# Performance work log

Hardware: AMD Instinct MI355X
Metric: run time of the kernel (lower is better)

The kernel has to match this reference:

```python
import jax, jax.numpy as jnp
from jax import lax
import numpy as np

EPS = 1e-5


def setup_inputs() -> dict:
    key = jax.random.key(0)
    ks = jax.random.split(key, 16)
    N, C, H, W = 8, 128, 128, 128
    MIP, OUP, K = 8, 128, 3
    inp = {}
    inp["x"] = jax.random.normal(ks[0], (N, C, H, W), dtype=jnp.float32)
    # conv1: 1x1, C -> MIP
    inp["w1"] = jax.random.normal(ks[1], (MIP, C), dtype=jnp.float32) * (1.0 / np.sqrt(C))
    inp["b1"] = jax.random.normal(ks[2], (MIP,), dtype=jnp.float32) * 0.02
    # bn1 (inference: frozen running stats)
    inp["g1"] = jnp.ones((MIP,), jnp.float32) + jax.random.normal(ks[3], (MIP,), jnp.float32) * 0.02
    inp["be1"] = jax.random.normal(ks[4], (MIP,), jnp.float32) * 0.02
    inp["m1"] = jax.random.normal(ks[5], (MIP,), jnp.float32) * 0.02
    inp["v1"] = jnp.ones((MIP,), jnp.float32)
    # conv_h / conv_w: 1x1, MIP -> C
    inp["wh"] = jax.random.normal(ks[6], (C, MIP), dtype=jnp.float32) * (1.0 / np.sqrt(MIP))
    inp["bh"] = jax.random.normal(ks[7], (C,), dtype=jnp.float32) * 0.02
    inp["ww"] = jax.random.normal(ks[8], (C, MIP), dtype=jnp.float32) * (1.0 / np.sqrt(MIP))
    inp["bw"] = jax.random.normal(ks[9], (C,), dtype=jnp.float32) * 0.02
    # final conv: KxK, C -> OUP
    inp["wc"] = jax.random.normal(ks[10], (OUP, C, K, K), dtype=jnp.float32) * (1.0 / np.sqrt(C * K * K))
    inp["bc"] = jax.random.normal(ks[11], (OUP,), dtype=jnp.float32) * 0.02
    inp["g2"] = jnp.ones((OUP,), jnp.float32) + jax.random.normal(ks[12], (OUP,), jnp.float32) * 0.02
    inp["be2"] = jax.random.normal(ks[13], (OUP,), jnp.float32) * 0.02
    inp["m2"] = jax.random.normal(ks[14], (OUP,), jnp.float32) * 0.02
    inp["v2"] = jnp.ones((OUP,), jnp.float32)
    return inp


def _bn1d(y, g, b, m, v):
    # y: (n, c, l); per-channel affine with frozen stats
    s = g / jnp.sqrt(v + EPS)
    return y * s[None, :, None] + (b - m * s)[None, :, None]


def _h_swish(y):
    return y * jnp.clip(y + 3.0, 0.0, 6.0) / 6.0


def reference(x, w1, b1, g1, be1, m1, v1, wh, bh, ww, bw, wc, bc, g2, be2, m2, v2):
    n, c, h, w = x.shape
    # Multi-scale pooled descriptors. Nearest interp of the 2-bin and 4-bin
    # adaptive pools back to length-1 picks bin 0, i.e. the mean over the
    # first half / first quarter of the pooled axis.
    x_h = x.mean(3) + x[..., : w // 2].mean(3) + x[..., : w // 4].mean(3)        # (n,c,h)
    x_w = x.mean(2) + x[:, :, : h // 2].mean(2) + x[:, :, : h // 4].mean(2)      # (n,c,w)
    y = jnp.concatenate([x_h, x_w], axis=2)                                       # (n,c,h+w)
    y = jnp.einsum('ncl,mc->nml', y, w1) + b1[None, :, None]                      # 1x1 conv
    y = _h_swish(_bn1d(y, g1, be1, m1, v1))
    xh, xw = y[:, :, :h], y[:, :, h:]
    a_h = jax.nn.sigmoid(jnp.einsum('nml,cm->ncl', xh, wh) + bh[None, :, None])[:, :, :, None]  # (n,c,h,1)
    a_w = jax.nn.sigmoid(jnp.einsum('nml,cm->ncl', xw, ww) + bw[None, :, None])[:, :, None, :]  # (n,c,1,w)
    out = x * a_w * a_h                                                           # gated features
    # final conv (kernel 3, stride 1, pad 1) + BN + SiLU
    out = lax.conv_general_dilated(out, wc, window_strides=(1, 1),
                                   padding=[(1, 1), (1, 1)],
                                   dimension_numbers=('NCHW', 'OIHW', 'NCHW'))
    out = out + bc[None, :, None, None]
    s2 = g2 / jnp.sqrt(v2 + EPS)
    out = out * s2[None, :, None, None] + (be2 - m2 * s2)[None, :, None, None]
    return out * jax.nn.sigmoid(out)
```

## Files before the change

kernel.cpp:

```cpp
#include <hip/hip_runtime.h>
#include <hip/hip_bf16.h>

typedef float f32x4 __attribute__((ext_vector_type(4)));
typedef __bf16 bf16x8 __attribute__((ext_vector_type(8)));

#define EPSF 1e-5f

__device__ __forceinline__ float pw(int i) {
    return (1.0f + (i < 64 ? 2.0f : 0.0f) + (i < 32 ? 4.0f : 0.0f)) * (1.0f / 128.0f);
}

__global__ __launch_bounds__(256) void pool_kernel(const float* __restrict__ x,
                                                   float* __restrict__ P) {
    int nc = blockIdx.x;
    const f32x4* plane = (const f32x4*)(x + (size_t)nc * 16384);
    __shared__ float rowpart[128][33];
    __shared__ __align__(16) f32x4 colpart[8][32];
    int t = threadIdx.x;
    int wq = t & 31, hg = t >> 5;
    f32x4 cacc = {0.f, 0.f, 0.f, 0.f};
    float u0 = pw(wq * 4), u1 = pw(wq * 4 + 1), u2 = pw(wq * 4 + 2), u3 = pw(wq * 4 + 3);
    #pragma unroll
    for (int j = 0; j < 16; ++j) {
        int r = hg * 16 + j;
        f32x4 v = plane[r * 32 + wq];
        rowpart[r][wq] = v.x * u0 + v.y * u1 + v.z * u2 + v.w * u3;
        cacc += v * pw(r);
    }
    colpart[hg][wq] = cacc;
    __syncthreads();
    float s = 0.f;
    if (t < 128) {
        #pragma unroll
        for (int q = 0; q < 32; ++q) s += rowpart[t][q];
        P[(size_t)nc * 256 + t] = s;
    } else {
        int w = t - 128;
        const float* cp = (const float*)colpart;
        #pragma unroll
        for (int g = 0; g < 8; ++g) s += cp[g * 128 + w];
        P[(size_t)nc * 256 + 128 + w] = s;
    }
}

__global__ __launch_bounds__(256) void attn_kernel(const float* __restrict__ P,
    const float* __restrict__ w1, const float* __restrict__ b1,
    const float* __restrict__ g1, const float* __restrict__ be1,
    const float* __restrict__ m1, const float* __restrict__ v1,
    const float* __restrict__ wh, const float* __restrict__ bh,
    const float* __restrict__ ww, const float* __restrict__ bw,
    float* __restrict__ A2) {
    int n = blockIdx.x >> 2, cg = blockIdx.x & 3, t = threadIdx.x;
    __shared__ float w1s[1024], whs[256], wws[256];
    __shared__ float bhs[32], bws[32];
    __shared__ float s1[8], t1[8], b1s[8];
    for (int i = t; i < 1024; i += 256) w1s[i] = w1[i];
    whs[t] = wh[cg * 256 + t];
    wws[t] = ww[cg * 256 + t];
    if (t < 32) { bhs[t] = bh[cg * 32 + t]; bws[t] = bw[cg * 32 + t]; }
    if (t < 8) {
        float s = g1[t] * rsqrtf(v1[t] + EPSF);
        s1[t] = s; t1[t] = be1[t] - m1[t] * s; b1s[t] = b1[t];
    }
    __syncthreads();
    float y[8];
    #pragma unroll
    for (int m = 0; m < 8; ++m) y[m] = b1s[m];
    const float* Pn = P + (size_t)n * 32768;
    for (int c = 0; c < 128; ++c) {
        float pv = Pn[c * 256 + t];
        #pragma unroll
        for (int m = 0; m < 8; ++m) y[m] += w1s[m * 128 + c] * pv;
    }
    #pragma unroll
    for (int m = 0; m < 8; ++m) {
        float v = y[m] * s1[m] + t1[m];
        float cl = fminf(fmaxf(v + 3.f, 0.f), 6.f);
        y[m] = v * cl * (1.f / 6.f);
    }
    const float* Ws_ = (t < 128) ? whs : wws;
    const float* Bs = (t < 128) ? bhs : bws;
    float* On = A2 + (size_t)n * 32768;
    for (int cc = 0; cc < 32; ++cc) {
        int c = cg * 32 + cc;
        float a = Bs[cc];
        #pragma unroll
        for (int m = 0; m < 8; ++m) a += y[m] * Ws_[cc * 8 + m];
        On[c * 256 + t] = 1.f / (1.f + __expf(-a));
    }
}

__global__ __launch_bounds__(256) void wtrans_kernel(const float* __restrict__ wc,
    const float* __restrict__ bc, const float* __restrict__ g2, const float* __restrict__ be2,
    const float* __restrict__ m2, const float* __restrict__ v2,
    __hip_bfloat16* __restrict__ Wt, float* __restrict__ ab) {
    int g = blockIdx.x * 256 + threadIdx.x;
    int step = g >> 12, rem = g & 4095;
    int o = rem >> 5, m = rem & 31;
    int slotp = m >> 3, j = m & 7;
    int u = slotp ^ ((o >> 1) & 3);
    int kidx = u * 8 + j;
    int khw = step >> 2, c32 = step & 3;
    int c = c32 * 32 + kidx;
    Wt[g] = __float2bfloat16(wc[(o * 128 + c) * 9 + khw]);
    if (g < 128) {
        float s2 = g2[g] * rsqrtf(v2[g] + EPSF);
        ab[g] = s2;
        ab[128 + g] = bc[g] * s2 + be2[g] - m2[g] * s2;
    }
}

__device__ __forceinline__ int ldsoff(int w, int c) {
    return w * 128 + ((((c >> 3) ^ ((w & 7) << 1)) << 3) | (c & 7));
}

__global__ __launch_bounds__(256) void amul_kernel(const float* __restrict__ x,
    const float* __restrict__ A2, __hip_bfloat16* __restrict__ Xpad) {
    int nh = blockIdx.x;
    int n = nh >> 7, h = nh & 127;
    int t = threadIdx.x;
    __shared__ __align__(16) __hip_bfloat16 T[16384];
    __shared__ float ahs[128];
    if (t < 128) ahs[t] = A2[(size_t)(n * 128 + t) * 256 + h];

    uint4 z = {0u, 0u, 0u, 0u};
    __hip_bfloat16* Xn = Xpad + (size_t)n * 16900 * 128;
    if (t < 32) {
        int wp = (t & 1) ? 129 : 0, cb2 = t >> 1;
        *(uint4*)(Xn + (size_t)((h + 1) * 130 + wp) * 128 + cb2 * 8) = z;
    }
    if (h == 0 || h == 127) {
        int hp = (h == 0) ? 0 : 129;
        for (int i = t; i < 2080; i += 256) {
            int wp = i >> 4, cb2 = i & 15;
            *(uint4*)(Xn + (size_t)(hp * 130 + wp) * 128 + cb2 * 8) = z;
        }
    }
    __syncthreads();

    const float* xr  = x + ((size_t)n * 128 * 128 + h) * 128;
    const float* awr = A2 + (size_t)n * 32768 + 128;
    #pragma unroll
    for (int j = 0; j < 16; ++j) {
        int item = j * 256 + t;
        int c = item >> 5, w4 = item & 31;
        f32x4 xv = *(const f32x4*)(xr + (size_t)c * 16384 + w4 * 4);
        f32x4 av = *(const f32x4*)(awr + c * 256 + w4 * 4);
        float ah = ahs[c];
        #pragma unroll
        for (int k = 0; k < 4; ++k) {
            float val = xv[k] * av[k] * ah;
            T[ldsoff(w4 * 4 + k, c)] = __float2bfloat16(val);
        }
    }
    __syncthreads();
    __hip_bfloat16* orow = Xn + (size_t)((h + 1) * 130 + 1) * 128;
    #pragma unroll
    for (int j = 0; j < 8; ++j) {
        int item = j * 256 + t;
        int w = item >> 4, cb = item & 15;
        int slot = cb ^ ((w & 7) << 1);
        uint4 v = *(const uint4*)&T[w * 128 + slot * 8];
        *(uint4*)(orow + w * 128 + cb * 8) = v;
    }
}

__global__ __launch_bounds__(512, 4) void conv_kernel(
    const __hip_bfloat16* __restrict__ Xpad, const __hip_bfloat16* __restrict__ Wt,
    const float* __restrict__ ab, float* __restrict__ out) {
    int bid = blockIdx.x;
    int work = (bid & 7) * 64 + (bid >> 3);
    int n = work >> 6, h0 = (work & 63) * 2;
    int tid = threadIdx.x;
    int lane = tid & 63, wid = tid >> 6;
    int wm = wid >> 2, wn = wid & 3;
    int r16 = lane & 15, u = lane >> 4;

    __shared__ __align__(16) __hip_bfloat16 Ws[3 * 4096];
    __shared__ __align__(16) __hip_bfloat16 Xs[3 * 8192];

    const __hip_bfloat16* Xn = Xpad + ((size_t)n * 16900 + (size_t)h0 * 130) * 128;

    int offA[4], offB[4];
    #pragma unroll
    for (int mi = 0; mi < 4; ++mi) {
        int o = wm * 64 + mi * 16 + r16;
        offA[mi] = o * 32 + ((u ^ ((o >> 1) & 3)) << 3);
    }
    #pragma unroll
    for (int ni = 0; ni < 4; ++ni) {
        int p = wn * 64 + ni * 16 + r16;
        offB[ni] = p * 32 + ((u ^ ((p >> 1) & 3)) << 3);
    }

    int xo[2];
    #pragma unroll
    for (int j = 0; j < 2; ++j) {
        int idx = j * 512 + tid, p = idx >> 2, s = idx & 3;
        int r2 = p >> 7, w = p & 127;
        xo[j] = (r2 * 130 + w) * 128 + ((s ^ ((p >> 1) & 3)) << 3);
    }

    auto stage = [&](int t) {
        int khw = t >> 2, c32 = t & 3;
        int kh = khw / 3, kw = khw - kh * 3;
        __builtin_amdgcn_global_load_lds(
            (const __attribute__((address_space(1))) void*)(Wt + t * 4096 + tid * 8),
            (__attribute__((address_space(3))) void*)(&Ws[(t % 3) * 4096 + tid * 8]),
            16, 0, 0);
        const __hip_bfloat16* xsrc = Xn + (kh * 130 + kw) * 128 + c32 * 32;
        __hip_bfloat16* xdst = &Xs[(t % 3) * 8192];
        #pragma unroll
        for (int j = 0; j < 2; ++j)
            __builtin_amdgcn_global_load_lds(
                (const __attribute__((address_space(1))) void*)(xsrc + xo[j]),
                (__attribute__((address_space(3))) void*)(xdst + (j * 512 + tid) * 8),
                16, 0, 0);
    };

    f32x4 acc[4][4];
    #pragma unroll
    for (int i = 0; i < 4; ++i)
        #pragma unroll
        for (int j = 0; j < 4; ++j) acc[i][j] = (f32x4){0.f, 0.f, 0.f, 0.f};

    stage(0);
    stage(1);
    asm volatile("s_waitcnt vmcnt(3)" ::: "memory");
    __builtin_amdgcn_sched_barrier(0);
    __builtin_amdgcn_s_barrier();
    __builtin_amdgcn_sched_barrier(0);

    #pragma unroll
    for (int t = 0; t < 36; ++t) {
        const __hip_bfloat16* Wb = &Ws[(t % 3) * 4096];
        const __hip_bfloat16* Xr = &Xs[(t % 3) * 8192];
        if (t + 2 < 36) stage(t + 2);

        bf16x8 xa[4], xb[4];
        #pragma unroll
        for (int mi = 0; mi < 4; ++mi) xa[mi] = *(const bf16x8*)&Wb[offA[mi]];
        #pragma unroll
        for (int ni = 0; ni < 4; ++ni) xb[ni] = *(const bf16x8*)&Xr[offB[ni]];
        asm volatile("s_waitcnt lgkmcnt(0)" ::: "memory");
        __builtin_amdgcn_sched_barrier(0);
        __builtin_amdgcn_s_setprio(1);
        #pragma unroll
        for (int mi = 0; mi < 4; ++mi)
            #pragma unroll
            for (int ni = 0; ni < 4; ++ni)
                acc[mi][ni] = __builtin_amdgcn_mfma_f32_16x16x32_bf16(
                    xa[mi], xb[ni], acc[mi][ni], 0, 0, 0);
        __builtin_amdgcn_s_setprio(0);

        if (t < 34) {
            asm volatile("s_waitcnt vmcnt(3)" ::: "memory");
        } else if (t == 34) {
            asm volatile("s_waitcnt vmcnt(0)" ::: "memory");
        }
        __builtin_amdgcn_sched_barrier(0);
        if (t < 35) {
            __builtin_amdgcn_s_barrier();
            __builtin_amdgcn_sched_barrier(0);
        }
    }

    #pragma unroll
    for (int mi = 0; mi < 4; ++mi) {
        #pragma unroll
        for (int r = 0; r < 4; ++r) {
            int o = wm * 64 + mi * 16 + u * 4 + r;
            float al = ab[o], be = ab[128 + o];
            size_t obase = (((size_t)n * 128 + o) * 128 + h0) * 128;
            #pragma unroll
            for (int ni = 0; ni < 4; ++ni) {
                int p = wn * 64 + ni * 16 + r16;
                int r2 = p >> 7, w = p & 127;
                float z = acc[mi][ni][r] * al + be;
                out[obase + r2 * 128 + w] = z / (1.f + __expf(-z));
            }
        }
    }
}

extern "C" void kernel_launch(void* const* d_in, const int* in_sizes, int n_in,
                              void* d_out, int out_size, void* d_ws, size_t ws_size,
                              hipStream_t stream) {
    const float* x   = (const float*)d_in[0];
    const float* w1  = (const float*)d_in[1];
    const float* b1  = (const float*)d_in[2];
    const float* g1  = (const float*)d_in[3];
    const float* be1 = (const float*)d_in[4];
    const float* m1  = (const float*)d_in[5];
    const float* v1  = (const float*)d_in[6];
    const float* wh  = (const float*)d_in[7];
    const float* bh  = (const float*)d_in[8];
    const float* ww  = (const float*)d_in[9];
    const float* bw  = (const float*)d_in[10];
    const float* wc  = (const float*)d_in[11];
    const float* bc  = (const float*)d_in[12];
    const float* g2  = (const float*)d_in[13];
    const float* be2 = (const float*)d_in[14];
    const float* m2  = (const float*)d_in[15];
    const float* v2  = (const float*)d_in[16];
    float* out = (float*)d_out;

    char* ws = (char*)d_ws;
    float* P  = (float*)(ws);
    float* A2 = (float*)(ws + (1 << 20));
    __hip_bfloat16* Xpad = (__hip_bfloat16*)(ws + (2 << 20));
    __hip_bfloat16* Wt   = (__hip_bfloat16*)(ws + (2 << 20) + 34611200);
    float* ab = (float*)(ws + (2 << 20) + 34611200 + 294912);

    pool_kernel<<<1024, 256, 0, stream>>>(x, P);
    attn_kernel<<<32, 256, 0, stream>>>(P, w1, b1, g1, be1, m1, v1, wh, bh, ww, bw, A2);
    wtrans_kernel<<<576, 256, 0, stream>>>(wc, bc, g2, be2, m2, v2, Wt, ab);
    amul_kernel<<<1024, 256, 0, stream>>>(x, A2, Xpad);
    conv_kernel<<<512, 512, 0, stream>>>(Xpad, Wt, ab, out);
}
```

Baseline: 110.0 us.

## Merge attn and weight-transform kernels; enlarge per-wave conv tile to 128x64

The conv kernel now runs 4 waves per block instead of 8, and each wave computes all 128 output channels for a 64-pixel slice. This doubles A-fragment register reuse and halves LDS fragment reads per MFMA, at the cost of more accumulator registers (128 VGPRs of acc) and fewer waves for latency hiding. Each thread also issues twice as many global-to-LDS loads, and the vmcnt waits are adjusted to match. Separately, the attention and weight-transform kernels are merged into one launch with a block-index split, removing one kernel launch.

```diff
diff --git a/kernel.cpp b/kernel.cpp
--- a/kernel.cpp
+++ b/kernel.cpp
@@ -43,14 +43,35 @@
     }
 }
 
-__global__ __launch_bounds__(256) void attn_kernel(const float* __restrict__ P,
+__global__ __launch_bounds__(256) void attn_wtrans_kernel(const float* __restrict__ P,
     const float* __restrict__ w1, const float* __restrict__ b1,
     const float* __restrict__ g1, const float* __restrict__ be1,
     const float* __restrict__ m1, const float* __restrict__ v1,
     const float* __restrict__ wh, const float* __restrict__ bh,
     const float* __restrict__ ww, const float* __restrict__ bw,
-    float* __restrict__ A2) {
-    int n = blockIdx.x >> 2, cg = blockIdx.x & 3, t = threadIdx.x;
+    const float* __restrict__ wc, const float* __restrict__ bc,
+    const float* __restrict__ g2, const float* __restrict__ be2,
+    const float* __restrict__ m2, const float* __restrict__ v2,
+    float* __restrict__ A2, __hip_bfloat16* __restrict__ Wt, float* __restrict__ ab) {
+    int t = threadIdx.x;
+    if (blockIdx.x >= 32) {
+        int g = (blockIdx.x - 32) * 256 + t;
+        int step = g >> 12, rem = g & 4095;
+        int o = rem >> 5, m = rem & 31;
+        int slotp = m >> 3, j = m & 7;
+        int u = slotp ^ ((o >> 1) & 3);
+        int kidx = u * 8 + j;
+        int khw = step >> 2, c32 = step & 3;
+        int c = c32 * 32 + kidx;
+        Wt[g] = __float2bfloat16(wc[(o * 128 + c) * 9 + khw]);
+        if (g < 128) {
+            float s2 = g2[g] * rsqrtf(v2[g] + EPSF);
+            ab[g] = s2;
+            ab[128 + g] = bc[g] * s2 + be2[g] - m2[g] * s2;
+        }
+        return;
+    }
+    int n = blockIdx.x >> 2, cg = blockIdx.x & 3;
     __shared__ float w1s[1024], whs[256], wws[256];
     __shared__ float bhs[32], bws[32];
     __shared__ float s1[8], t1[8], b1s[8];
@@ -90,26 +111,6 @@
     }
 }
 
-__global__ __launch_bounds__(256) void wtrans_kernel(const float* __restrict__ wc,
-    const float* __restrict__ bc, const float* __restrict__ g2, const float* __restrict__ be2,
-    const float* __restrict__ m2, const float* __restrict__ v2,
-    __hip_bfloat16* __restrict__ Wt, float* __restrict__ ab) {
-    int g = blockIdx.x * 256 + threadIdx.x;
-    int step = g >> 12, rem = g & 4095;
-    int o = rem >> 5, m = rem & 31;
-    int slotp = m >> 3, j = m & 7;
-    int u = slotp ^ ((o >> 1) & 3);
-    int kidx = u * 8 + j;
-    int khw = step >> 2, c32 = step & 3;
-    int c = c32 * 32 + kidx;
-    Wt[g] = __float2bfloat16(wc[(o * 128 + c) * 9 + khw]);
-    if (g < 128) {
-        float s2 = g2[g] * rsqrtf(v2[g] + EPSF);
-        ab[g] = s2;
-        ab[128 + g] = bc[g] * s2 + be2[g] - m2[g] * s2;
-    }
-}
-
 __device__ __forceinline__ int ldsoff(int w, int c) {
     return w * 128 + ((((c >> 3) ^ ((w & 7) << 1)) << 3) | (c & 7));
 }
@@ -165,15 +166,15 @@
     }
 }
 
-__global__ __launch_bounds__(512, 4) void conv_kernel(
+__global__ __launch_bounds__(256, 2) void conv_kernel(
     const __hip_bfloat16* __restrict__ Xpad, const __hip_bfloat16* __restrict__ Wt,
     const float* __restrict__ ab, float* __restrict__ out) {
     int bid = blockIdx.x;
     int work = (bid & 7) * 64 + (bid >> 3);
     int n = work >> 6, h0 = (work & 63) * 2;
     int tid = threadIdx.x;
-    int lane = tid & 63, wid = tid >> 6;
-    int wm = wid >> 2, wn = wid & 3;
+    int lane = tid & 63;
+    int wn = tid >> 6;
     int r16 = lane & 15, u = lane >> 4;
 
     __shared__ __align__(16) __hip_bfloat16 Ws[3 * 4096];
@@ -181,10 +182,10 @@
 
     const __hip_bfloat16* Xn = Xpad + ((size_t)n * 16900 + (size_t)h0 * 130) * 128;
 
-    int offA[4], offB[4];
-    #pragma unroll
-    for (int mi = 0; mi < 4; ++mi) {
-        int o = wm * 64 + mi * 16 + r16;
+    int offA[8], offB[4];
+    #pragma unroll
+    for (int mi = 0; mi < 8; ++mi) {
+        int o = mi * 16 + r16;
         offA[mi] = o * 32 + ((u ^ ((o >> 1) & 3)) << 3);
     }
     #pragma unroll
@@ -193,10 +194,10 @@
         offB[ni] = p * 32 + ((u ^ ((p >> 1) & 3)) << 3);
     }
 
-    int xo[2];
-    #pragma unroll
-    for (int j = 0; j < 2; ++j) {
-        int idx = j * 512 + tid, p = idx >> 2, s = idx & 3;
+    int xo[4];
+    #pragma unroll
+    for (int j = 0; j < 4; ++j) {
+        int idx = j * 256 + tid, p = idx >> 2, s = idx & 3;
         int r2 = p >> 7, w = p & 127;
         xo[j] = (r2 * 130 + w) * 128 + ((s ^ ((p >> 1) & 3)) << 3);
     }
@@ -204,29 +205,31 @@
     auto stage = [&](int t) {
         int khw = t >> 2, c32 = t & 3;
         int kh = khw / 3, kw = khw - kh * 3;
-        __builtin_amdgcn_global_load_lds(
-            (const __attribute__((address_space(1))) void*)(Wt + t * 4096 + tid * 8),
-            (__attribute__((address_space(3))) void*)(&Ws[(t % 3) * 4096 + tid * 8]),
-            16, 0, 0);
+        #pragma unroll
+        for (int j = 0; j < 2; ++j)
+            __builtin_amdgcn_global_load_lds(
+                (const __attribute__((address_space(1))) void*)(Wt + t * 4096 + (j * 256 + tid) * 8),
+                (__attribute__((address_space(3))) void*)(&Ws[(t % 3) * 4096 + (j * 256 + tid) * 8]),
+                16, 0, 0);
         const __hip_bfloat16* xsrc = Xn + (kh * 130 + kw) * 128 + c32 * 32;
         __hip_bfloat16* xdst = &Xs[(t % 3) * 8192];
         #pragma unroll
-        for (int j = 0; j < 2; ++j)
+        for (int j = 0; j < 4; ++j)
             __builtin_amdgcn_global_load_lds(
                 (const __attribute__((address_space(1))) void*)(xsrc + xo[j]),
-                (__attribute__((address_space(3))) void*)(xdst + (j * 512 + tid) * 8),
+                (__attribute__((address_space(3))) void*)(xdst + (j * 256 + tid) * 8),
                 16, 0, 0);
     };
 
-    f32x4 acc[4][4];
-    #pragma unroll
-    for (int i = 0; i < 4; ++i)
+    f32x4 acc[8][4];
+    #pragma unroll
+    for (int i = 0; i < 8; ++i)
         #pragma unroll
         for (int j = 0; j < 4; ++j) acc[i][j] = (f32x4){0.f, 0.f, 0.f, 0.f};
 
     stage(0);
     stage(1);
-    asm volatile("s_waitcnt vmcnt(3)" ::: "memory");
+    asm volatile("s_waitcnt vmcnt(6)" ::: "memory");
     __builtin_amdgcn_sched_barrier(0);
     __builtin_amdgcn_s_barrier();
     __builtin_amdgcn_sched_barrier(0);
@@ -237,24 +240,24 @@
         const __hip_bfloat16* Xr = &Xs[(t % 3) * 8192];
         if (t + 2 < 36) stage(t + 2);
 
-        bf16x8 xa[4], xb[4];
-        #pragma unroll
-        for (int mi = 0; mi < 4; ++mi) xa[mi] = *(const bf16x8*)&Wb[offA[mi]];
-        #pragma unroll
-        for (int ni = 0; ni < 4; ++ni) xb[ni] = *(const bf16x8*)&Xr[offB[ni]];
+        bf16x8 fa[8], fb[4];
+        #pragma unroll
+        for (int mi = 0; mi < 8; ++mi) fa[mi] = *(const bf16x8*)&Wb[offA[mi]];
+        #pragma unroll
+        for (int ni = 0; ni < 4; ++ni) fb[ni] = *(const bf16x8*)&Xr[offB[ni]];
         asm volatile("s_waitcnt lgkmcnt(0)" ::: "memory");
         __builtin_amdgcn_sched_barrier(0);
         __builtin_amdgcn_s_setprio(1);
         #pragma unroll
-        for (int mi = 0; mi < 4; ++mi)
+        for (int mi = 0; mi < 8; ++mi)
             #pragma unroll
             for (int ni = 0; ni < 4; ++ni)
                 acc[mi][ni] = __builtin_amdgcn_mfma_f32_16x16x32_bf16(
-                    xa[mi], xb[ni], acc[mi][ni], 0, 0, 0);
+                    fa[mi], fb[ni], acc[mi][ni], 0, 0, 0);
         __builtin_amdgcn_s_setprio(0);
 
         if (t < 34) {
-            asm volatile("s_waitcnt vmcnt(3)" ::: "memory");
+            asm volatile("s_waitcnt vmcnt(6)" ::: "memory");
         } else if (t == 34) {
             asm volatile("s_waitcnt vmcnt(0)" ::: "memory");
         }
@@ -266,10 +269,10 @@
     }
 
     #pragma unroll
-    for (int mi = 0; mi < 4; ++mi) {
+    for (int mi = 0; mi < 8; ++mi) {
         #pragma unroll
         for (int r = 0; r < 4; ++r) {
-            int o = wm * 64 + mi * 16 + u * 4 + r;
+            int o = mi * 16 + u * 4 + r;
             float al = ab[o], be = ab[128 + o];
             size_t obase = (((size_t)n * 128 + o) * 128 + h0) * 128;
             #pragma unroll
@@ -313,8 +316,9 @@
     float* ab = (float*)(ws + (2 << 20) + 34611200 + 294912);
 
     pool_kernel<<<1024, 256, 0, stream>>>(x, P);
-    attn_kernel<<<32, 256, 0, stream>>>(P, w1, b1, g1, be1, m1, v1, wh, bh, ww, bw, A2);
-    wtrans_kernel<<<576, 256, 0, stream>>>(wc, bc, g2, be2, m2, v2, Wt, ab);
+    attn_wtrans_kernel<<<608, 256, 0, stream>>>(P, w1, b1, g1, be1, m1, v1,
+                                                wh, bh, ww, bw, wc, bc, g2, be2, m2, v2,
+                                                A2, Wt, ab);
     amul_kernel<<<1024, 256, 0, stream>>>(x, A2, Xpad);
-    conv_kernel<<<512, 512, 0, stream>>>(Xpad, Wt, ab, out);
-}
+    conv_kernel<<<512, 256, 0, stream>>>(Xpad, Wt, ab, out);
+}
```

Measured after the change: 109.9 us. Within noise of the previous version (-0.0%).
